# Kernel optimization log

Hardware: AMD Instinct MI355X
Metric: run time of the kernel (lower is better)

Reference implementation:

```python
import jax, jax.numpy as jnp
import numpy as np

B = 256        # graphs per batch (python loop in original, vectorized here)
N = 512        # nodes per graph
DEG = 16       # avg degree
E_PER = N * DEG
T = 64         # num_node_types
D = 128        # gnn_hidden_dim


def setup_inputs() -> dict:
    key = jax.random.key(0)
    ks = jax.random.split(key, 8)
    node_feat = jax.random.randint(ks[0], (B * N,), 0, T)
    offs = (jnp.arange(B) * N)[:, None]
    src = (jax.random.randint(ks[1], (B, E_PER), 0, N) + offs).reshape(-1)
    dst = (jax.random.randint(ks[2], (B, E_PER), 0, N) + offs).reshape(-1)
    emb_table = jax.random.normal(ks[3], (T, D), dtype=jnp.float32) * 0.02
    W1 = jax.random.normal(ks[4], (D, D), dtype=jnp.float32) * (1.0 / np.sqrt(D))
    b1 = jnp.zeros((D,), dtype=jnp.float32)
    W2 = jax.random.normal(ks[5], (D, D), dtype=jnp.float32) * (1.0 / np.sqrt(D))
    b2 = jnp.zeros((D,), dtype=jnp.float32)
    return {"node_feat": node_feat, "src": src, "dst": dst,
            "emb_table": emb_table, "W1": W1, "b1": b1, "W2": W2, "b2": b2}


def _gcn_layer(h, src, dst, out_isqrt, in_isqrt, W, b, n):
    # DGL GraphConv, norm='both': D_in^{-1/2} A D_out^{-1/2} h W + b
    m = (h * out_isqrt[:, None])[src]                      # [E, D] gather
    agg = jax.ops.segment_sum(m, dst, num_segments=n)      # [Ntot, D] scatter
    return (agg * in_isqrt[:, None]) @ W + b


def reference(node_feat, src, dst, emb_table, W1, b1, W2, b2):
    n = node_feat.shape[0]
    ones = jnp.ones(src.shape[0], dtype=emb_table.dtype)
    deg_out = jnp.clip(jax.ops.segment_sum(ones, src, num_segments=n), 1.0)
    deg_in = jnp.clip(jax.ops.segment_sum(ones, dst, num_segments=n), 1.0)
    out_isqrt = jax.lax.rsqrt(deg_out)
    in_isqrt = jax.lax.rsqrt(deg_in)

    h = emb_table[node_feat]                                # [Ntot, D]
    # layer 1 (dropout is eval-mode identity) + relu, layer 2 + relu
    h = jax.nn.relu(_gcn_layer(h, src, dst, out_isqrt, in_isqrt, W1, b1, n))
    h = jax.nn.relu(_gcn_layer(h, src, dst, out_isqrt, in_isqrt, W2, b2, n))

    # dgl.mean_nodes per graph, then mean_gnn_embeddings + stack -> [B, D]
    gid = jnp.arange(n) // N
    hg = jax.ops.segment_sum(h, gid, num_segments=B) / float(N)
    return hg
```

## Files before the change

kernel.cpp:

```cpp
#include <hip/hip_runtime.h>
#include <stdint.h>

#define GRAPHS 256
#define NPG    512
#define EPG    8192
#define NTOT   (GRAPHS*NPG)

typedef __attribute__((ext_vector_type(8))) short s16x8;
typedef __attribute__((ext_vector_type(4))) float f32x4;

__device__ __forceinline__ float bf2f(unsigned short u){
  union { unsigned int i; float f; } c; c.i = ((unsigned int)u)<<16; return c.f;
}
__device__ __forceinline__ unsigned short f2bf(float f){
  union { float f; unsigned int i; } c; c.f = f;
  unsigned int r = c.i + 0x7fffu + ((c.i>>16)&1u);
  return (unsigned short)(r>>16);
}

__global__ __launch_bounds__(512) void k_csr(const int* __restrict__ src,
      const int* __restrict__ dst, const int* __restrict__ ntype,
      const float* __restrict__ emb, const float* __restrict__ W1,
      unsigned short* __restrict__ sorted_g, int* __restrict__ start_g,
      float* __restrict__ out_isqrt, unsigned short* __restrict__ EW1T){
  __shared__ int hist[NPG], cursor[NPG], co[NPG], cs[NPG+1];
  __shared__ unsigned short ntype_sh[NPG];
  __shared__ unsigned short sorted[EPG];
  const int tid=threadIdx.x;
  if (blockIdx.x >= GRAPHS){
    const int gid = (blockIdx.x-GRAPHS)*512 + tid;
    const int t = gid>>7, c = gid&127;
    float acc=0.f;
    #pragma unroll 4
    for (int k=0;k<128;k++) acc += emb[t*128+k]*W1[k*128+c];
    EW1T[c*64+t]=f2bf(acc);
    return;
  }
  const int b=blockIdx.x, eb=b*EPG, nb=b*NPG;
  hist[tid]=0; co[tid]=0; ntype_sh[tid]=(unsigned short)ntype[nb+tid];
  __syncthreads();
  int4 d4[4], s4[4];
  {
    const int4* dv = (const int4*)(dst+eb);
    const int4* sv = (const int4*)(src+eb);
    #pragma unroll
    for (int j=0;j<4;j++){
      d4[j]=dv[tid + j*512];
      s4[j]=sv[tid + j*512];
      atomicAdd(&hist[d4[j].x&(NPG-1)],1); atomicAdd(&hist[d4[j].y&(NPG-1)],1);
      atomicAdd(&hist[d4[j].z&(NPG-1)],1); atomicAdd(&hist[d4[j].w&(NPG-1)],1);
      atomicAdd(&co[s4[j].x&(NPG-1)],1);   atomicAdd(&co[s4[j].y&(NPG-1)],1);
      atomicAdd(&co[s4[j].z&(NPG-1)],1);   atomicAdd(&co[s4[j].w&(NPG-1)],1);
    }
  }
  __syncthreads();
  if (tid<64){
    int carry=0;
    #pragma unroll
    for (int c=0;c<8;c++){
      int sc=hist[64*c+tid];
      #pragma unroll
      for (int off=1;off<64;off<<=1){ int y=__shfl_up(sc,off); if (tid>=off) sc+=y; }
      cs[64*c+tid+1]=carry+sc;
      carry+=__shfl(sc,63);
    }
    if (tid==0) cs[0]=0;
  }
  __syncthreads();
  cursor[tid]=cs[tid];
  __syncthreads();
  #pragma unroll
  for (int j=0;j<4;j++){
    int dl, s, pos;
    dl=d4[j].x&(NPG-1); s=s4[j].x&(NPG-1);
    pos=atomicAdd(&cursor[dl],1); sorted[pos]=(unsigned short)((ntype_sh[s]<<9)|s);
    dl=d4[j].y&(NPG-1); s=s4[j].y&(NPG-1);
    pos=atomicAdd(&cursor[dl],1); sorted[pos]=(unsigned short)((ntype_sh[s]<<9)|s);
    dl=d4[j].z&(NPG-1); s=s4[j].z&(NPG-1);
    pos=atomicAdd(&cursor[dl],1); sorted[pos]=(unsigned short)((ntype_sh[s]<<9)|s);
    dl=d4[j].w&(NPG-1); s=s4[j].w&(NPG-1);
    pos=atomicAdd(&cursor[dl],1); sorted[pos]=(unsigned short)((ntype_sh[s]<<9)|s);
  }
  __syncthreads();
  for (int i=tid;i<EPG/2;i+=512)
    ((unsigned int*)(sorted_g+(size_t)eb))[i] = ((const unsigned int*)sorted)[i];
  if (tid==0) start_g[b*(NPG+1)+NPG]=cs[NPG];
  start_g[b*(NPG+1)+tid]=cs[tid];
  {
    int a=co[tid]; if(a<1)a=1;
    out_isqrt[nb+tid]=rsqrtf((float)a);
  }
}

#define A1_LDS 73232
__global__ __launch_bounds__(512) void k_agg1(
      const unsigned short* __restrict__ sorted_g, const int* __restrict__ start_g,
      const unsigned short* __restrict__ EW1T, const float* __restrict__ out_isqrt,
      const float* __restrict__ b1, unsigned short* __restrict__ h1F){
  extern __shared__ char smem[];
  float* S      = (float*)(smem);
  float* wsc    = (float*)(smem + 69632);
  int*   sstart = (int*)  (smem + 71680);
  float* bsh    = (float*)(smem + 72720);
  const int bid=blockIdx.x, b=bid>>1, half=bid&1;
  const int v0=half*256, nb=b*NPG, tid=threadIdx.x;
  for (int i=tid; i<(256*68)/4; i+=512) ((f32x4*)S)[i]=(f32x4){0.f,0.f,0.f,0.f};
  for (int i=tid; i<NPG; i+=512) wsc[i]=out_isqrt[nb+i];
  for (int i=tid; i<257; i+=512) sstart[i]=start_g[b*(NPG+1)+v0+i];
  if (tid<128) bsh[tid]=b1[tid];
  __syncthreads();
  if (tid<256){
    const int beg=sstart[tid], end=sstart[tid+1];
    float* Sd = S + tid*68;
    const unsigned short* sg = sorted_g + (size_t)b*EPG;
    for (int i=beg;i<end;++i){
      const int ent = sg[i];
      Sd[ent>>9] += wsc[ent&511];
    }
  }
  __syncthreads();
  const int wave=tid>>6, lane=tid&63, l16=lane&15, quad=lane>>4;
  f32x4 acc[2][8];
  #pragma unroll
  for (int rt=0;rt<2;rt++)
    #pragma unroll
    for (int nt=0;nt<8;nt++) acc[rt][nt]=(f32x4){0.f,0.f,0.f,0.f};
  #pragma unroll
  for (int ks=0; ks<4; ++ks){
    const int kc = (ks&1)*32 + quad*8;
    s16x8 a[2];
    #pragma unroll
    for (int rt=0;rt<2;rt++){
      const int m = (wave*2+rt)*16 + l16;
      const float* sp = &S[m*68 + kc];
      f32x4 va = *(const f32x4*)sp;
      f32x4 vb = *(const f32x4*)(sp+4);
      union { s16x8 v; unsigned short u[8]; } pk;
      #pragma unroll
      for (int j=0;j<8;j++){
        const float f = (j<4)? va[j] : vb[j-4];
        const unsigned short hi = f2bf(f);
        pk.u[j] = (ks<2) ? hi : f2bf(f - bf2f(hi));
      }
      a[rt]=pk.v;
    }
    #pragma unroll
    for (int nt=0;nt<8;nt++){
      s16x8 bfr=__builtin_bit_cast(s16x8,
          *(const uint4*)(EW1T + (size_t)(nt*16+l16)*64 + kc));
      #pragma unroll
      for (int rt=0;rt<2;rt++)
        acc[rt][nt]=__builtin_amdgcn_mfma_f32_16x16x32_bf16(a[rt],bfr,acc[rt][nt],0,0,0);
    }
  }
  #pragma unroll
  for (int rt=0;rt<2;rt++){
    const int W = wave*2+rt;
    const int mloc = W*16 + quad*4;
    float isq[4], os[4];
    #pragma unroll
    for (int r=0;r<4;r++){
      int d = sstart[mloc+r+1]-sstart[mloc+r]; if (d<1) d=1;
      isq[r]=rsqrtf((float)d);
      os[r]=wsc[v0+mloc+r];
    }
    const int ks2 = half*8 + (W>>1);
    const int q2  = ((W&1)<<1) | (quad>>1);
    const int j0  = (quad&1)*4;
    #pragma unroll
    for (int nt=0;nt<8;nt++){
      const int col = nt*16+l16;
      const float bb = bsh[col];
      ushort4 st;
      float v;
      v = fmaxf(acc[rt][nt][0]*isq[0]+bb,0.f)*os[0]; st.x=f2bf(v);
      v = fmaxf(acc[rt][nt][1]*isq[1]+bb,0.f)*os[1]; st.y=f2bf(v);
      v = fmaxf(acc[rt][nt][2]*isq[2]+bb,0.f)*os[2]; st.z=f2bf(v);
      v = fmaxf(acc[rt][nt][3]*isq[3]+bb,0.f)*os[3]; st.w=f2bf(v);
      const size_t off = ((((size_t)b*16 + ks2)*8 + nt)*64 + q2*16 + l16)*8 + j0;
      *(ushort4*)(h1F + off) = st;
    }
  }
}

#define A2_LDS 67080
__global__ __launch_bounds__(512) void k_agg2(
      const unsigned short* __restrict__ sorted_g, const int* __restrict__ start_g,
      const unsigned short* __restrict__ h1F, unsigned short* __restrict__ M1F){
  extern __shared__ char smem[];
  unsigned char* A = (unsigned char*)smem;
  unsigned int* A32 = (unsigned int*)smem;
  int* sstart = (int*)(smem + 66560);
  const int bid=blockIdx.x;
  const int b  = ((bid>>5)<<3) | (bid&7);
  const int dt = (bid>>3)&3;
  const int v0=dt*128, tid=threadIdx.x;
  for (int i=tid; i<66560/16; i+=512) ((uint4*)smem)[i]=(uint4){0u,0u,0u,0u};
  for (int i=tid; i<129; i+=512) sstart[i]=start_g[b*(NPG+1)+v0+i];
  __syncthreads();
  {
    const int d = tid>>2, q = tid&3;
    const int beg=sstart[d], end=sstart[d+1], len=end-beg;
    const int qb = beg + ((len*q)>>2), qe = beg + ((len*(q+1))>>2);
    const unsigned short* sg = sorted_g + (size_t)b*EPG;
    const int rowbase = d*130;
    for (int i=qb;i<qe;++i){
      const int s = sg[i]&511;
      atomicAdd(&A32[rowbase + (s>>2)], 1u<<((s&3)*8));
    }
  }
  __syncthreads();
  const int wave=tid>>6, lane=tid&63, l16=lane&15, quad=lane>>4;
  const int mg=wave>>1, ng=wave&1;
  f32x4 acc[2][4];
  #pragma unroll
  for (int rt=0;rt<2;rt++)
    #pragma unroll
    for (int ct=0;ct<4;ct++) acc[rt][ct]=(f32x4){0.f,0.f,0.f,0.f};

  const uint4* bp[4];
  #pragma unroll
  for (int ct=0;ct<4;ct++)
    bp[ct] = (const uint4*)h1F + (((size_t)b*16)*8 + (ng*4+ct))*64 + lane;
  const unsigned char* Ab[2];
  #pragma unroll
  for (int rt=0;rt<2;rt++)
    Ab[rt] = A + ((mg*2+rt)*16 + l16)*520 + quad*8;

  #pragma unroll 2
  for (int ks=0; ks<16; ++ks){
    uint4 bq[4];
    #pragma unroll
    for (int ct=0;ct<4;ct++) bq[ct] = bp[ct][(size_t)ks*512];
    s16x8 afr[2];
    #pragma unroll
    for (int rt=0;rt<2;rt++){
      const uint2 aw = *(const uint2*)(Ab[rt] + ks*32);
      union { s16x8 v; unsigned short u[8]; } pk;
      #pragma unroll
      for (int j=0;j<4;j++){
        const float f0 = (float)((aw.x>>(8*j))&0xffu);
        const float f1 = (float)((aw.y>>(8*j))&0xffu);
        pk.u[j]   = (unsigned short)(__builtin_bit_cast(unsigned int, f0)>>16);
        pk.u[j+4] = (unsigned short)(__builtin_bit_cast(unsigned int, f1)>>16);
      }
      afr[rt]=pk.v;
    }
    #pragma unroll
    for (int rt=0;rt<2;rt++)
      #pragma unroll
      for (int ct=0;ct<4;ct++)
        acc[rt][ct]=__builtin_amdgcn_mfma_f32_16x16x32_bf16(afr[rt],
            __builtin_bit_cast(s16x8, bq[ct]), acc[rt][ct],0,0,0);
  }
  #pragma unroll
  for (int rt=0;rt<2;rt++){
    const int mloc=(mg*2+rt)*16 + quad*4;
    const int M = dt*8 + mg*2 + rt;
    float isq[4];
    #pragma unroll
    for (int r=0;r<4;r++){
      int d=sstart[mloc+r+1]-sstart[mloc+r]; if (d<1) d=1;
      isq[r]=rsqrtf((float)d);
    }
    #pragma unroll
    for (int ct=0;ct<4;ct++){
      const int ks2   = ng*2 + (ct>>1);
      const int quad2 = ((ct&1)<<1) | (l16>>3);
      const int j     = l16&7;
      unsigned short* base = M1F
          + ((((size_t)b*32+M)*4+ks2)*64 + quad2*16)*8 + j;
      #pragma unroll
      for (int r=0;r<4;r++)
        base[(size_t)(quad*4+r)*8] = f2bf(acc[rt][ct][r]*isq[r]);
    }
  }
}

__global__ __launch_bounds__(512) void k_gemm2(const unsigned short* __restrict__ M1F,
      const float* __restrict__ W2, const float* __restrict__ b2,
      float* __restrict__ out){
  __shared__ __align__(16) unsigned short WT[128][136];
  __shared__ float bsh[128];
  __shared__ float colpart[8][128];
  const int b=blockIdx.x, tid=threadIdx.x;
  for (int idx=tid; idx<128*128; idx+=512){
    const int k=idx>>7, n=idx&127;
    WT[n][k]=f2bf(W2[idx]);
  }
  if (tid<128) bsh[tid]=b2[tid];
  __syncthreads();
  const int wave=tid>>6, lane=tid&63, l16=lane&15, quad=lane>>4;
  float p[8];
  #pragma unroll
  for (int i=0;i<8;i++) p[i]=0.f;
  for (int chunk=0; chunk<2; ++chunk){
    f32x4 acc[2][8];
    #pragma unroll
    for (int rt=0;rt<2;rt++)
      #pragma unroll
      for (int ct=0;ct<8;ct++) acc[rt][ct]=(f32x4){0.f,0.f,0.f,0.f};
    #pragma unroll
    for (int ks=0;ks<4;ks++){
      s16x8 a[2], bf[8];
      #pragma unroll
      for (int rt=0;rt<2;rt++){
        const int M = wave*4 + chunk*2 + rt;
        a[rt]=__builtin_bit_cast(s16x8, *(const uint4*)(M1F
            + ((((size_t)b*32+M)*4+ks)*64 + lane)*8));
      }
      #pragma unroll
      for (int ct=0;ct<8;ct++)
        bf[ct]=__builtin_bit_cast(s16x8, *(const uint4*)&WT[ct*16+l16][ks*32+quad*8]);
      #pragma unroll
      for (int rt=0;rt<2;rt++)
        #pragma unroll
        for (int ct=0;ct<8;ct++)
          acc[rt][ct]=__builtin_amdgcn_mfma_f32_16x16x32_bf16(a[rt],bf[ct],acc[rt][ct],0,0,0);
    }
    #pragma unroll
    for (int rt=0;rt<2;rt++)
      #pragma unroll
      for (int ct=0;ct<8;ct++)
        #pragma unroll
        for (int r=0;r<4;r++){
          const int col=ct*16+l16;
          p[ct] += fmaxf(acc[rt][ct][r]+bsh[col],0.f);
        }
  }
  #pragma unroll
  for (int ct=0;ct<8;ct++){
    p[ct] += __shfl_xor(p[ct],16);
    p[ct] += __shfl_xor(p[ct],32);
  }
  if (quad==0){
    #pragma unroll
    for (int ct=0;ct<8;ct++) colpart[wave][ct*16+l16]=p[ct];
  }
  __syncthreads();
  if (tid<128){
    float s=0.f;
    #pragma unroll
    for (int w=0;w<8;w++) s+=colpart[w][tid];
    out[b*128+tid]=s*(1.f/512.f);
  }
}

extern "C" void kernel_launch(void* const* d_in, const int* in_sizes, int n_in,
                              void* d_out, int out_size, void* d_ws, size_t ws_size,
                              hipStream_t stream){
  const int* node_feat = (const int*)d_in[0];
  const int* src = (const int*)d_in[1];
  const int* dst = (const int*)d_in[2];
  const float* emb = (const float*)d_in[3];
  const float* W1  = (const float*)d_in[4];
  const float* b1  = (const float*)d_in[5];
  const float* W2  = (const float*)d_in[6];
  const float* b2  = (const float*)d_in[7];

  char* ws = (char*)d_ws;
  float* out_isqrt        = (float*)(ws);
  int* start_g            = (int*)(ws + 524288);
  unsigned short* sorted_g= (unsigned short*)(ws + 1049600);
  unsigned short* EW1T    = (unsigned short*)(ws + 5243904);
  unsigned short* h1F     = (unsigned short*)(ws + 5260288);
  unsigned short* M1F     = (unsigned short*)(ws + 38814720);

  (void)hipFuncSetAttribute(reinterpret_cast<const void*>(&k_agg1),
        hipFuncAttributeMaxDynamicSharedMemorySize, A1_LDS);
  (void)hipFuncSetAttribute(reinterpret_cast<const void*>(&k_agg2),
        hipFuncAttributeMaxDynamicSharedMemorySize, A2_LDS);

  k_csr<<<GRAPHS+16,512,0,stream>>>(src,dst,node_feat,emb,W1,
        sorted_g,start_g,out_isqrt,EW1T);
  k_agg1<<<GRAPHS*2,512,A1_LDS,stream>>>(sorted_g,start_g,EW1T,out_isqrt,b1,h1F);
  k_agg2<<<GRAPHS*4,512,A2_LDS,stream>>>(sorted_g,start_g,h1F,M1F);
  k_gemm2<<<GRAPHS,512,0,stream>>>(M1F,W2,b2,(float*)d_out);
}
```

Baseline: 150.0 us.

## Fuse CSR build, emb·W1 product and layer-1 aggregation into one kernel

Merges the CSR construction kernel and the first aggregation kernel into a single per-graph kernel. Each block recomputes the emb_table·W1 product into shared memory, and the sorted edges, degrees and out-norms stay in LDS instead of going through global memory. This removes a kernel launch, the round-trip of sorted_g/out_isqrt/EW1T, and the grid dependency between the two stages. In exchange every block redoes the 64x128x128 product, LDS use grows to about 107 KB, which limits occupancy, and the grid for layer 1 halves to 256 blocks that process both halves serially.

After: 155.2 us. 3.5% more time.

```diff
diff --git a/kernel.cpp b/kernel.cpp
--- a/kernel.cpp
+++ b/kernel.cpp
@@ -18,50 +18,66 @@
   return (unsigned short)(r>>16);
 }
 
-__global__ __launch_bounds__(512) void k_csr(const int* __restrict__ src,
+#define BUILD_LDS 109568
+__global__ __launch_bounds__(512) void k_build(const int* __restrict__ src,
       const int* __restrict__ dst, const int* __restrict__ ntype,
       const float* __restrict__ emb, const float* __restrict__ W1,
-      unsigned short* __restrict__ sorted_g, int* __restrict__ start_g,
-      float* __restrict__ out_isqrt, unsigned short* __restrict__ EW1T){
-  __shared__ int hist[NPG], cursor[NPG], co[NPG], cs[NPG+1];
-  __shared__ unsigned short ntype_sh[NPG];
-  __shared__ unsigned short sorted[EPG];
-  const int tid=threadIdx.x;
-  if (blockIdx.x >= GRAPHS){
-    const int gid = (blockIdx.x-GRAPHS)*512 + tid;
-    const int t = gid>>7, c = gid&127;
-    float acc=0.f;
-    #pragma unroll 4
-    for (int k=0;k<128;k++) acc += emb[t*128+k]*W1[k*128+c];
-    EW1T[c*64+t]=f2bf(acc);
-    return;
-  }
-  const int b=blockIdx.x, eb=b*EPG, nb=b*NPG;
+      const float* __restrict__ b1, unsigned short* __restrict__ sorted_g,
+      int* __restrict__ start_g, unsigned short* __restrict__ h1F){
+  extern __shared__ char smem[];
+  float* S        = (float*)(smem);
+  int*   hist     = (int*)(smem);
+  int*   co       = (int*)(smem + 2048);
+  int*   cursor   = (int*)(smem + 4096);
+  unsigned short* ntype_sh = (unsigned short*)(smem + 6144);
+  float* emb_sh   = (float*)(smem + 8192);
+  unsigned short* sorted = (unsigned short*)(smem + 69632);
+  unsigned short* ew     = (unsigned short*)(smem + 86016);
+  int*   cs       = (int*)(smem + 104448);
+  float* wsc      = (float*)(smem + 106504);
+  float* bsh      = (float*)(smem + 108552);
+  const int b=blockIdx.x, tid=threadIdx.x, eb=b*EPG, nb=b*NPG;
+
   hist[tid]=0; co[tid]=0; ntype_sh[tid]=(unsigned short)ntype[nb+tid];
-  __syncthreads();
+  for (int i=tid; i<8192/4; i+=512) ((f32x4*)emb_sh)[i]=((const f32x4*)emb)[i];
+  if (tid<128) bsh[tid]=b1[tid];
   int4 d4[4], s4[4];
   {
     const int4* dv = (const int4*)(dst+eb);
     const int4* sv = (const int4*)(src+eb);
     #pragma unroll
-    for (int j=0;j<4;j++){
-      d4[j]=dv[tid + j*512];
-      s4[j]=sv[tid + j*512];
-      atomicAdd(&hist[d4[j].x&(NPG-1)],1); atomicAdd(&hist[d4[j].y&(NPG-1)],1);
-      atomicAdd(&hist[d4[j].z&(NPG-1)],1); atomicAdd(&hist[d4[j].w&(NPG-1)],1);
-      atomicAdd(&co[s4[j].x&(NPG-1)],1);   atomicAdd(&co[s4[j].y&(NPG-1)],1);
-      atomicAdd(&co[s4[j].z&(NPG-1)],1);   atomicAdd(&co[s4[j].w&(NPG-1)],1);
-    }
+    for (int j=0;j<4;j++){ d4[j]=dv[tid + j*512]; s4[j]=sv[tid + j*512]; }
+  }
+  __syncthreads();
+  {
+    const int c = tid&127, tg = tid>>7;
+    float acc[16];
+    #pragma unroll
+    for (int i=0;i<16;i++) acc[i]=0.f;
+    for (int k=0;k<128;k++){
+      const float w1 = W1[k*128+c];
+      #pragma unroll
+      for (int i=0;i<16;i++) acc[i] += emb_sh[(tg*16+i)*128 + k]*w1;
+    }
+    #pragma unroll
+    for (int i=0;i<16;i++) ew[c*72 + tg*16+i] = f2bf(acc[i]);
+  }
+  #pragma unroll
+  for (int j=0;j<4;j++){
+    atomicAdd(&hist[d4[j].x&(NPG-1)],1); atomicAdd(&hist[d4[j].y&(NPG-1)],1);
+    atomicAdd(&hist[d4[j].z&(NPG-1)],1); atomicAdd(&hist[d4[j].w&(NPG-1)],1);
+    atomicAdd(&co[s4[j].x&(NPG-1)],1);   atomicAdd(&co[s4[j].y&(NPG-1)],1);
+    atomicAdd(&co[s4[j].z&(NPG-1)],1);   atomicAdd(&co[s4[j].w&(NPG-1)],1);
   }
   __syncthreads();
   if (tid<64){
     int carry=0;
     #pragma unroll
-    for (int c=0;c<8;c++){
-      int sc=hist[64*c+tid];
+    for (int c2=0;c2<8;c2++){
+      int sc=hist[64*c2+tid];
       #pragma unroll
       for (int off=1;off<64;off<<=1){ int y=__shfl_up(sc,off); if (tid>=off) sc+=y; }
-      cs[64*c+tid+1]=carry+sc;
+      cs[64*c2+tid+1]=carry+sc;
       carry+=__shfl(sc,63);
     }
     if (tid==0) cs[0]=0;
@@ -84,101 +100,90 @@
   __syncthreads();
   for (int i=tid;i<EPG/2;i+=512)
     ((unsigned int*)(sorted_g+(size_t)eb))[i] = ((const unsigned int*)sorted)[i];
+  start_g[b*(NPG+1)+tid]=cs[tid];
   if (tid==0) start_g[b*(NPG+1)+NPG]=cs[NPG];
-  start_g[b*(NPG+1)+tid]=cs[tid];
   {
     int a=co[tid]; if(a<1)a=1;
-    out_isqrt[nb+tid]=rsqrtf((float)a);
-  }
-}
-
-#define A1_LDS 73232
-__global__ __launch_bounds__(512) void k_agg1(
-      const unsigned short* __restrict__ sorted_g, const int* __restrict__ start_g,
-      const unsigned short* __restrict__ EW1T, const float* __restrict__ out_isqrt,
-      const float* __restrict__ b1, unsigned short* __restrict__ h1F){
-  extern __shared__ char smem[];
-  float* S      = (float*)(smem);
-  float* wsc    = (float*)(smem + 69632);
-  int*   sstart = (int*)  (smem + 71680);
-  float* bsh    = (float*)(smem + 72720);
-  const int bid=blockIdx.x, b=bid>>1, half=bid&1;
-  const int v0=half*256, nb=b*NPG, tid=threadIdx.x;
-  for (int i=tid; i<(256*68)/4; i+=512) ((f32x4*)S)[i]=(f32x4){0.f,0.f,0.f,0.f};
-  for (int i=tid; i<NPG; i+=512) wsc[i]=out_isqrt[nb+i];
-  for (int i=tid; i<257; i+=512) sstart[i]=start_g[b*(NPG+1)+v0+i];
-  if (tid<128) bsh[tid]=b1[tid];
-  __syncthreads();
-  if (tid<256){
-    const int beg=sstart[tid], end=sstart[tid+1];
-    float* Sd = S + tid*68;
-    const unsigned short* sg = sorted_g + (size_t)b*EPG;
-    for (int i=beg;i<end;++i){
-      const int ent = sg[i];
-      Sd[ent>>9] += wsc[ent&511];
-    }
-  }
-  __syncthreads();
+    wsc[tid]=rsqrtf((float)a);
+  }
+  __syncthreads();
+
   const int wave=tid>>6, lane=tid&63, l16=lane&15, quad=lane>>4;
-  f32x4 acc[2][8];
-  #pragma unroll
-  for (int rt=0;rt<2;rt++)
-    #pragma unroll
-    for (int nt=0;nt<8;nt++) acc[rt][nt]=(f32x4){0.f,0.f,0.f,0.f};
-  #pragma unroll
-  for (int ks=0; ks<4; ++ks){
-    const int kc = (ks&1)*32 + quad*8;
-    s16x8 a[2];
+  for (int half=0; half<2; ++half){
+    const int v0=half*256;
+    __syncthreads();
+    for (int i=tid; i<(256*68)/4; i+=512) ((f32x4*)S)[i]=(f32x4){0.f,0.f,0.f,0.f};
+    __syncthreads();
+    if (tid<256){
+      const int d = v0 + tid;
+      const int beg=cs[d], end=cs[d+1];
+      float* Sd = S + tid*68;
+      for (int i=beg;i<end;++i){
+        const int ent = sorted[i];
+        Sd[ent>>9] += wsc[ent&511];
+      }
+    }
+    __syncthreads();
+    f32x4 acc[2][8];
+    #pragma unroll
+    for (int rt=0;rt<2;rt++)
+      #pragma unroll
+      for (int nt=0;nt<8;nt++) acc[rt][nt]=(f32x4){0.f,0.f,0.f,0.f};
+    #pragma unroll
+    for (int ks=0; ks<4; ++ks){
+      const int kc = (ks&1)*32 + quad*8;
+      s16x8 a[2];
+      #pragma unroll
+      for (int rt=0;rt<2;rt++){
+        const int m = (wave*2+rt)*16 + l16;
+        const float* sp = &S[m*68 + kc];
+        f32x4 va = *(const f32x4*)sp;
+        f32x4 vb = *(const f32x4*)(sp+4);
+        union { s16x8 v; unsigned short u[8]; } pk;
+        #pragma unroll
+        for (int j=0;j<8;j++){
+          const float f = (j<4)? va[j] : vb[j-4];
+          const unsigned short hi = f2bf(f);
+          pk.u[j] = (ks<2) ? hi : f2bf(f - bf2f(hi));
+        }
+        a[rt]=pk.v;
+      }
+      #pragma unroll
+      for (int nt=0;nt<8;nt++){
+        s16x8 bfr=__builtin_bit_cast(s16x8,
+            *(const uint4*)(ew + (nt*16+l16)*72 + kc));
+        #pragma unroll
+        for (int rt=0;rt<2;rt++)
+          acc[rt][nt]=__builtin_amdgcn_mfma_f32_16x16x32_bf16(a[rt],bfr,acc[rt][nt],0,0,0);
+      }
+    }
     #pragma unroll
     for (int rt=0;rt<2;rt++){
-      const int m = (wave*2+rt)*16 + l16;
-      const float* sp = &S[m*68 + kc];
-      f32x4 va = *(const f32x4*)sp;
-      f32x4 vb = *(const f32x4*)(sp+4);
-      union { s16x8 v; unsigned short u[8]; } pk;
-      #pragma unroll
-      for (int j=0;j<8;j++){
-        const float f = (j<4)? va[j] : vb[j-4];
-        const unsigned short hi = f2bf(f);
-        pk.u[j] = (ks<2) ? hi : f2bf(f - bf2f(hi));
-      }
-      a[rt]=pk.v;
-    }
-    #pragma unroll
-    for (int nt=0;nt<8;nt++){
-      s16x8 bfr=__builtin_bit_cast(s16x8,
-          *(const uint4*)(EW1T + (size_t)(nt*16+l16)*64 + kc));
-      #pragma unroll
-      for (int rt=0;rt<2;rt++)
-        acc[rt][nt]=__builtin_amdgcn_mfma_f32_16x16x32_bf16(a[rt],bfr,acc[rt][nt],0,0,0);
-    }
-  }
-  #pragma unroll
-  for (int rt=0;rt<2;rt++){
-    const int W = wave*2+rt;
-    const int mloc = W*16 + quad*4;
-    float isq[4], os[4];
-    #pragma unroll
-    for (int r=0;r<4;r++){
-      int d = sstart[mloc+r+1]-sstart[mloc+r]; if (d<1) d=1;
-      isq[r]=rsqrtf((float)d);
-      os[r]=wsc[v0+mloc+r];
-    }
-    const int ks2 = half*8 + (W>>1);
-    const int q2  = ((W&1)<<1) | (quad>>1);
-    const int j0  = (quad&1)*4;
-    #pragma unroll
-    for (int nt=0;nt<8;nt++){
-      const int col = nt*16+l16;
-      const float bb = bsh[col];
-      ushort4 st;
-      float v;
-      v = fmaxf(acc[rt][nt][0]*isq[0]+bb,0.f)*os[0]; st.x=f2bf(v);
-      v = fmaxf(acc[rt][nt][1]*isq[1]+bb,0.f)*os[1]; st.y=f2bf(v);
-      v = fmaxf(acc[rt][nt][2]*isq[2]+bb,0.f)*os[2]; st.z=f2bf(v);
-      v = fmaxf(acc[rt][nt][3]*isq[3]+bb,0.f)*os[3]; st.w=f2bf(v);
-      const size_t off = ((((size_t)b*16 + ks2)*8 + nt)*64 + q2*16 + l16)*8 + j0;
-      *(ushort4*)(h1F + off) = st;
+      const int W = wave*2+rt;
+      const int mloc = W*16 + quad*4;
+      float isq[4], os[4];
+      #pragma unroll
+      for (int r=0;r<4;r++){
+        int d = cs[v0+mloc+r+1]-cs[v0+mloc+r]; if (d<1) d=1;
+        isq[r]=rsqrtf((float)d);
+        os[r]=wsc[v0+mloc+r];
+      }
+      const int ks2 = half*8 + (W>>1);
+      const int q2  = ((W&1)<<1) | (quad>>1);
+      const int j0  = (quad&1)*4;
+      #pragma unroll
+      for (int nt=0;nt<8;nt++){
+        const int col = nt*16+l16;
+        const float bb = bsh[col];
+        ushort4 st;
+        float v;
+        v = fmaxf(acc[rt][nt][0]*isq[0]+bb,0.f)*os[0]; st.x=f2bf(v);
+        v = fmaxf(acc[rt][nt][1]*isq[1]+bb,0.f)*os[1]; st.y=f2bf(v);
+        v = fmaxf(acc[rt][nt][2]*isq[2]+bb,0.f)*os[2]; st.z=f2bf(v);
+        v = fmaxf(acc[rt][nt][3]*isq[3]+bb,0.f)*os[3]; st.w=f2bf(v);
+        const size_t off = ((((size_t)b*16 + ks2)*8 + nt)*64 + q2*16 + l16)*8 + j0;
+        *(ushort4*)(h1F + off) = st;
+      }
     }
   }
 }
@@ -217,7 +222,6 @@
   for (int rt=0;rt<2;rt++)
     #pragma unroll
     for (int ct=0;ct<4;ct++) acc[rt][ct]=(f32x4){0.f,0.f,0.f,0.f};
-
   const uint4* bp[4];
   #pragma unroll
   for (int ct=0;ct<4;ct++)
@@ -226,7 +230,6 @@
   #pragma unroll
   for (int rt=0;rt<2;rt++)
     Ab[rt] = A + ((mg*2+rt)*16 + l16)*520 + quad*8;
-
   #pragma unroll 2
   for (int ks=0; ks<16; ++ks){
     uint4 bq[4];
@@ -359,21 +362,18 @@
   const float* b2  = (const float*)d_in[7];
 
   char* ws = (char*)d_ws;
-  float* out_isqrt        = (float*)(ws);
-  int* start_g            = (int*)(ws + 524288);
-  unsigned short* sorted_g= (unsigned short*)(ws + 1049600);
-  unsigned short* EW1T    = (unsigned short*)(ws + 5243904);
-  unsigned short* h1F     = (unsigned short*)(ws + 5260288);
-  unsigned short* M1F     = (unsigned short*)(ws + 38814720);
-
-  (void)hipFuncSetAttribute(reinterpret_cast<const void*>(&k_agg1),
-        hipFuncAttributeMaxDynamicSharedMemorySize, A1_LDS);
+  int* start_g            = (int*)(ws);
+  unsigned short* sorted_g= (unsigned short*)(ws + 525312);
+  unsigned short* h1F     = (unsigned short*)(ws + 4719616);
+  unsigned short* M1F     = (unsigned short*)(ws + 38274048);
+
+  (void)hipFuncSetAttribute(reinterpret_cast<const void*>(&k_build),
+        hipFuncAttributeMaxDynamicSharedMemorySize, BUILD_LDS);
   (void)hipFuncSetAttribute(reinterpret_cast<const void*>(&k_agg2),
         hipFuncAttributeMaxDynamicSharedMemorySize, A2_LDS);
 
-  k_csr<<<GRAPHS+16,512,0,stream>>>(src,dst,node_feat,emb,W1,
-        sorted_g,start_g,out_isqrt,EW1T);
-  k_agg1<<<GRAPHS*2,512,A1_LDS,stream>>>(sorted_g,start_g,EW1T,out_isqrt,b1,h1F);
+  k_build<<<GRAPHS,512,BUILD_LDS,stream>>>(src,dst,node_feat,emb,W1,b1,
+        sorted_g,start_g,h1F);
   k_agg2<<<GRAPHS*4,512,A2_LDS,stream>>>(sorted_g,start_g,h1F,M1F);
   k_gemm2<<<GRAPHS,512,0,stream>>>(M1F,W2,b2,(float*)d_out);
 }
```
